# Performance work log

Hardware: AMD Instinct MI355X
Metric: run time of the kernel (lower is better)

## Reference

```python
import jax, jax.numpy as jnp
import numpy as np

EMB_DIM = 768
NUM_HEADS = 12
HEAD_DIM = EMB_DIM // NUM_HEADS
B, S = 8, 1024


def setup_inputs() -> dict:
    key = jax.random.key(0)
    ks = jax.random.split(key, 8)
    q = jax.random.normal(ks[0], (B, S, EMB_DIM), dtype=jnp.float32)
    k = jax.random.normal(ks[1], (B, S, EMB_DIM), dtype=jnp.float32)
    v = jax.random.normal(ks[2], (B, S, EMB_DIM), dtype=jnp.float32)
    # Per-head projection weights, torch nn.Linear layout [out_dim, in_dim]
    xav = float(np.sqrt(6.0 / (HEAD_DIM + HEAD_DIM)))
    Wq = jax.random.uniform(ks[3], (NUM_HEADS, HEAD_DIM, HEAD_DIM), jnp.float32, -xav, xav)
    Wk = jax.random.uniform(ks[4], (NUM_HEADS, HEAD_DIM, HEAD_DIM), jnp.float32, -xav, xav)
    Wv = jax.random.uniform(ks[5], (NUM_HEADS, HEAD_DIM, HEAD_DIM), jnp.float32, -xav, xav)
    # Output projection (torch Linear default init scale not critical for correctness baseline)
    bound = float(1.0 / np.sqrt(EMB_DIM))
    Wo = jax.random.uniform(ks[6], (EMB_DIM, EMB_DIM), jnp.float32, -bound, bound)
    bo = jax.random.uniform(ks[7], (EMB_DIM,), jnp.float32, -bound, bound)
    return {"q": q, "k": k, "v": v, "Wq": Wq, "Wk": Wk, "Wv": Wv, "Wo": Wo, "bo": bo}


def reference(q, k, v, Wq, Wk, Wv, Wo, bo):
    b, s, _ = q.shape
    # split heads: [B, S, E] -> [B, H, S, d]
    def split(x):
        return x.reshape(b, s, NUM_HEADS, HEAD_DIM).transpose(0, 2, 1, 3)
    qh, kh, vh = split(q), split(k), split(v)
    # per-head linear (torch: y = x @ W^T), vectorized over heads
    Q = jnp.einsum('bhsd,hod->bhso', qh, Wq)
    K = jnp.einsum('bhsd,hod->bhso', kh, Wk)
    V = jnp.einsum('bhsd,hod->bhso', vh, Wv)
    scale = 1.0 / jnp.sqrt(jnp.float32(HEAD_DIM))
    scores = jnp.einsum('bhqd,bhkd->bhqk', Q, K) * scale  # [B,H,S,S]
    weights = jax.nn.softmax(scores, axis=-1)
    attn = jnp.einsum('bhqk,bhkd->bhqd', weights, V)
    # merge heads: [B,H,S,d] -> [B,S,E]
    attn = attn.transpose(0, 2, 1, 3).reshape(b, s, EMB_DIM)
    return attn @ Wo.T + bo
```

## Files before the change

kernel.cpp:

```cpp
#include <hip/hip_runtime.h>
#include <hip/hip_bf16.h>

#define BB 8
#define SS 1024
#define EE 768
#define HH 12
#define DD 64
#define NT (BB*SS)

typedef __attribute__((ext_vector_type(8))) short bf16x8;
typedef __attribute__((ext_vector_type(4))) float f32x4;

__device__ __forceinline__ ushort f2bf(float f) {
  union { float f; unsigned u; } x; x.f = f;
  unsigned r = x.u + 0x7fffu + ((x.u >> 16) & 1u);
  return (ushort)(r >> 16);
}

__device__ __forceinline__ unsigned cvtpk(float a, float b) {
  unsigned r;
  asm("v_cvt_pk_bf16_f32 %0, %1, %2" : "=v"(r) : "v"(a), "v"(b));
  return r;
}

__device__ __forceinline__ void gl2lds(const void* g, void* l) {
  __builtin_amdgcn_global_load_lds(
      (const __attribute__((address_space(1))) unsigned int*)g,
      (__attribute__((address_space(3))) unsigned int*)l, 16, 0, 0);
}

#define MFMA16(A, B, C) __builtin_amdgcn_mfma_f32_16x16x32_bf16((A), (B), (C), 0, 0, 0)

__global__ void cvt_weights(const float* __restrict__ Wq, const float* __restrict__ Wk,
                            const float* __restrict__ Wv, const float* __restrict__ Wo,
                            ushort* __restrict__ Wqb, ushort* __restrict__ Wkb,
                            ushort* __restrict__ Wvb, ushort* __restrict__ Wob) {
  int i = blockIdx.x * blockDim.x + threadIdx.x;
  const int NW = HH*DD*DD;
  if (i < NW) { Wqb[i] = f2bf(Wq[i]); Wkb[i] = f2bf(Wk[i]); Wvb[i] = f2bf(Wv[i]); }
  if (i < EE*EE) Wob[i] = f2bf(Wo[i]);
}

__global__ __launch_bounds__(256) void proj_qkv(
    const float* __restrict__ q, const float* __restrict__ k, const float* __restrict__ v,
    const ushort* __restrict__ Wqb, const ushort* __restrict__ Wkb, const ushort* __restrict__ Wvb,
    ushort* __restrict__ Qb, ushort* __restrict__ Kb, ushort* __restrict__ Vt) {
  int bid = blockIdx.x;
  int m  = bid / (BB*HH*4);
  int r  = bid % (BB*HH*4);
  int bh = r % (BB*HH);
  int tg = r / (BB*HH);
  int b = bh / HH, h = bh % HH;

  int tid = threadIdx.x;
  int w = tid >> 6, l = tid & 63;
  int lr = l & 15, lg = l >> 4;

  const float*  xbase = (m==0 ? q : (m==1 ? k : v))
                      + ((size_t)(b*SS + tg*256 + w*16 + lr))*EE + h*DD;
  const ushort* W = (m==0 ? Wqb : (m==1 ? Wkb : Wvb)) + h*DD*DD;

  bf16x8 wb0[4], wb1[4];
#pragma unroll
  for (int f = 0; f < 4; ++f) {
    wb0[f] = *(const bf16x8*)(W + (f*16 + lr)*DD + lg*8);
    wb1[f] = *(const bf16x8*)(W + (f*16 + lr)*DD + 32 + lg*8);
  }

  f32x4 nx0 = *(const f32x4*)(xbase + lg*8);
  f32x4 nx1 = *(const f32x4*)(xbase + lg*8 + 4);
  f32x4 nx2 = *(const f32x4*)(xbase + 32 + lg*8);
  f32x4 nx3 = *(const f32x4*)(xbase + 36 + lg*8);

  float qscale = (m == 0) ? 0.18033688011112042f : 1.0f;

#pragma unroll
  for (int t = 0; t < 4; ++t) {
    f32x4 c0 = nx0, c1 = nx1, c2 = nx2, c3 = nx3;
    if (t < 3) {
      const float* xn = xbase + (size_t)(t + 1)*64*EE;
      nx0 = *(const f32x4*)(xn + lg*8);
      nx1 = *(const f32x4*)(xn + lg*8 + 4);
      nx2 = *(const f32x4*)(xn + 32 + lg*8);
      nx3 = *(const f32x4*)(xn + 36 + lg*8);
    }
    union { bf16x8 v; unsigned u[4]; } a0, a1;
    a0.u[0] = cvtpk(c0[0], c0[1]); a0.u[1] = cvtpk(c0[2], c0[3]);
    a0.u[2] = cvtpk(c1[0], c1[1]); a0.u[3] = cvtpk(c1[2], c1[3]);
    a1.u[0] = cvtpk(c2[0], c2[1]); a1.u[1] = cvtpk(c2[2], c2[3]);
    a1.u[2] = cvtpk(c3[0], c3[1]); a1.u[3] = cvtpk(c3[2], c3[3]);

    f32x4 acc[4] = {};
    int st = tg*4 + t;
    if (m == 2) {
#pragma unroll
      for (int f = 0; f < 4; ++f) {
        acc[f] = MFMA16(a0.v, wb0[f], acc[f]);
        acc[f] = MFMA16(a1.v, wb1[f], acc[f]);
      }
      int posb = st*64 + 32*(w>>1) + 8*lg + 4*(w&1);
#pragma unroll
      for (int f = 0; f < 4; ++f) {
        ushort2 p0, p1;
        *(unsigned*)&p0 = cvtpk(acc[f][0], acc[f][1]);
        *(unsigned*)&p1 = cvtpk(acc[f][2], acc[f][3]);
        ushort4 pk; pk.x = p0.x; pk.y = p0.y; pk.z = p1.x; pk.w = p1.y;
        *(ushort4*)(Vt + ((size_t)bh*DD + f*16 + lr)*SS + posb) = pk;
      }
    } else {
#pragma unroll
      for (int f = 0; f < 4; ++f) {
        acc[f] = MFMA16(wb0[f], a0.v, acc[f]);
        acc[f] = MFMA16(wb1[f], a1.v, acc[f]);
      }
      ushort* dst = (m == 0 ? Qb : Kb) + ((size_t)bh*SS + st*64 + w*16 + lr)*DD;
#pragma unroll
      for (int f = 0; f < 4; ++f) {
        ushort2 p0, p1;
        *(unsigned*)&p0 = cvtpk(acc[f][0]*qscale, acc[f][1]*qscale);
        *(unsigned*)&p1 = cvtpk(acc[f][2]*qscale, acc[f][3]*qscale);
        ushort4 pk; pk.x = p0.x; pk.y = p0.y; pk.z = p1.x; pk.w = p1.y;
        *(ushort4*)(dst + f*16 + lg*4) = pk;
      }
    }
  }
}

__global__ __launch_bounds__(256) void attn_fwd(
    const ushort* __restrict__ Qb, const ushort* __restrict__ Kb,
    const ushort* __restrict__ Vt, ushort* __restrict__ attn) {
  __shared__ uint4 ldsq[2560];
  char* ldsb = (char*)ldsq;

  int bid = blockIdx.x;
  int bh = bid % (BB*HH);
  int qt = bid / (BB*HH);
  int b = bh / HH, h = bh % HH;
  int tid = threadIdx.x, w = tid >> 6, l = tid & 63;
  int lr = l & 15, lg = l >> 4;

  const ushort* Qp0 = Qb + ((size_t)bh*SS + qt*128 + w*32 + lr)*DD;
  bf16x8 bq[2][2];
  bq[0][0] = *(const bf16x8*)(Qp0 + lg*8);
  bq[0][1] = *(const bf16x8*)(Qp0 + 32 + lg*8);
  bq[1][0] = *(const bf16x8*)(Qp0 + 16*DD + lg*8);
  bq[1][1] = *(const bf16x8*)(Qp0 + 16*DD + 32 + lg*8);

  const ushort* Kbh = Kb + (size_t)bh*SS*DD;
  const ushort* Vbh = Vt + (size_t)bh*DD*SS;

  const short ONE = (short)0x3F80;
  bf16x8 ones = {ONE, ONE, ONE, ONE, ONE, ONE, ONE, ONE};

  f32x4 lsum[2] = {};
  f32x4 o[2][4] = {};

#define STAGE_K(kbuf, kt) do {                                                   \
    char* KB_ = ldsb + (kbuf)*8192;                                              \
    const ushort* ksrc = Kbh + ((size_t)((kt)*64 + w*16 + lr))*DD + lg*8;        \
    gl2lds(ksrc,      KB_ + tid*16);                                             \
    gl2lds(ksrc + 32, KB_ + 4096 + tid*16);                                      \
  } while (0)
#define STAGE_V(vbuf, kt) do {                                                   \
    char* VB_ = ldsb + 24576 + (vbuf)*8192;                                      \
    const ushort* vsrc = Vbh + ((size_t)(w*16 + lr))*SS + (kt)*64 + lg*8;        \
    gl2lds(vsrc,      VB_ + tid*16);                                             \
    gl2lds(vsrc + 32, VB_ + 4096 + tid*16);                                      \
  } while (0)

  STAGE_K(0, 0);
  STAGE_V(0, 0);
  STAGE_K(1, 1);
  int kbuf = 0, vbuf = 0;
  for (int kt = 0; kt < 16; ++kt) {
    const char* KB_ = ldsb + kbuf*8192;
    const char* VB_ = ldsb + 24576 + vbuf*8192;

    if (kt < 15) { asm volatile("s_waitcnt vmcnt(2)" ::: "memory"); }
    else         { asm volatile("s_waitcnt vmcnt(0)" ::: "memory"); }
    __builtin_amdgcn_s_barrier();
    __builtin_amdgcn_sched_barrier(0);

    if (kt < 15) STAGE_V(vbuf ^ 1, kt + 1);
    if (kt < 14) { int nk = kbuf + 2; if (nk >= 3) nk -= 3; STAGE_K(nk, kt + 2); }

    f32x4 st0[4] = {}, st1[4] = {};
    __builtin_amdgcn_s_setprio(1);
#pragma unroll
    for (int f = 0; f < 4; ++f) {
      bf16x8 k0 = *(const bf16x8*)(KB_ + f*1024 + l*16);
      bf16x8 k1 = *(const bf16x8*)(KB_ + 4096 + f*1024 + l*16);
      st0[f] = MFMA16(k0, bq[0][0], st0[f]);
      st0[f] = MFMA16(k1, bq[0][1], st0[f]);
      st1[f] = MFMA16(k0, bq[1][0], st1[f]);
      st1[f] = MFMA16(k1, bq[1][1], st1[f]);
    }
    __builtin_amdgcn_s_setprio(0);

    union { bf16x8 v; unsigned u[4]; } pba[2], pbb[2];
#pragma unroll
    for (int s = 0; s < 2; ++s) {
      f32x4* st = (s == 0) ? st0 : st1;
#pragma unroll
      for (int f = 0; f < 4; ++f) {
#pragma unroll
        for (int j = 0; j < 4; ++j) st[f][j] = __builtin_amdgcn_exp2f(st[f][j]);
      }
      pba[s].u[0] = cvtpk(st[0][0], st[0][1]); pba[s].u[1] = cvtpk(st[0][2], st[0][3]);
      pba[s].u[2] = cvtpk(st[1][0], st[1][1]); pba[s].u[3] = cvtpk(st[1][2], st[1][3]);
      pbb[s].u[0] = cvtpk(st[2][0], st[2][1]); pbb[s].u[1] = cvtpk(st[2][2], st[2][3]);
      pbb[s].u[2] = cvtpk(st[3][0], st[3][1]); pbb[s].u[3] = cvtpk(st[3][2], st[3][3]);
    }

    __builtin_amdgcn_s_setprio(1);
#pragma unroll
    for (int f = 0; f < 4; ++f) {
      bf16x8 va = *(const bf16x8*)(VB_ + f*1024 + l*16);
      bf16x8 vc = *(const bf16x8*)(VB_ + 4096 + f*1024 + l*16);
      o[0][f] = MFMA16(va, pba[0].v, o[0][f]);
      o[0][f] = MFMA16(vc, pbb[0].v, o[0][f]);
      o[1][f] = MFMA16(va, pba[1].v, o[1][f]);
      o[1][f] = MFMA16(vc, pbb[1].v, o[1][f]);
    }
    lsum[0] = MFMA16(ones, pba[0].v, lsum[0]);
    lsum[0] = MFMA16(ones, pbb[0].v, lsum[0]);
    lsum[1] = MFMA16(ones, pba[1].v, lsum[1]);
    lsum[1] = MFMA16(ones, pbb[1].v, lsum[1]);
    __builtin_amdgcn_s_setprio(0);

    kbuf = (kbuf == 2) ? 0 : kbuf + 1;
    vbuf ^= 1;
  }
#undef STAGE_K
#undef STAGE_V

#pragma unroll
  for (int s = 0; s < 2; ++s) {
    float inv = 1.0f / lsum[s][0];
    ushort* orow = attn + ((size_t)(b*SS + qt*128 + w*32 + s*16 + lr))*EE + h*DD;
#pragma unroll
    for (int f = 0; f < 4; ++f) {
      ushort4 pkd;
      pkd.x = f2bf(o[s][f][0] * inv);
      pkd.y = f2bf(o[s][f][1] * inv);
      pkd.z = f2bf(o[s][f][2] * inv);
      pkd.w = f2bf(o[s][f][3] * inv);
      *(ushort4*)(orow + f*16 + lg*4) = pkd;
    }
  }
}

__global__ __launch_bounds__(256) void out_proj(
    const ushort* __restrict__ attn, const ushort* __restrict__ Wob,
    const float* __restrict__ bo, float* __restrict__ out) {
  __shared__ uint4 ldsq[3072];
  char* ldsb = (char*)ldsq;

  int bid = blockIdx.x;
  int mt = bid & 127;
  int nt = bid >> 7;
  int tid = threadIdx.x, w = tid >> 6, l = tid & 63;
  int lr = l & 15, lg = l >> 4;

  int rS = tid >> 3;
  int cSw = (((tid & 7) * 16) ^ ((rS & 7) << 4)) >> 1;

  const ushort* Abase = attn + ((size_t)mt*64)*EE;
  const ushort* Bbase = Wob + ((size_t)nt*128)*EE;

#define OSTAGE(bufidx, kt) do {                                                  \
    char* LA_ = ldsb + (bufidx)*24576;                                           \
    char* LB_ = LA_ + 8192;                                                      \
    const ushort* asrc = Abase + (kt)*64 + cSw;                                  \
    const ushort* bsrc = Bbase + (kt)*64 + cSw;                                  \
    gl2lds(asrc + (size_t)rS*EE,        LA_ + tid*16);                           \
    gl2lds(asrc + (size_t)(rS+32)*EE,   LA_ + 4096 + tid*16);                    \
    gl2lds(bsrc + (size_t)rS*EE,        LB_ + tid*16);                           \
    gl2lds(bsrc + (size_t)(rS+32)*EE,   LB_ + 4096 + tid*16);                    \
    gl2lds(bsrc + (size_t)(rS+64)*EE,   LB_ + 8192 + tid*16);                    \
    gl2lds(bsrc + (size_t)(rS+96)*EE,   LB_ + 12288 + tid*16);                   \
  } while (0)

  f32x4 acc[4][2] = {};

#define OCOMPUTE(bufidx) do {                                                    \
    const char* LA_ = ldsb + (bufidx)*24576;                                     \
    const char* LB_ = LA_ + 8192;                                                \
    bf16x8 af[4][2], bf[2][2];                                                   \
    _Pragma("unroll")                                                            \
    for (int f = 0; f < 4; ++f) {                                                \
      int row = f*16 + lr; int sw = (row & 7) << 4;                              \
      af[f][0] = *(const bf16x8*)(LA_ + row*128 + ((lg*16) ^ sw));               \
      af[f][1] = *(const bf16x8*)(LA_ + row*128 + ((64 + lg*16) ^ sw));          \
    }                                                                            \
    _Pragma("unroll")                                                            \
    for (int g = 0; g < 2; ++g) {                                                \
      int row = w*32 + g*16 + lr; int sw = (row & 7) << 4;                       \
      bf[g][0] = *(const bf16x8*)(LB_ + row*128 + ((lg*16) ^ sw));               \
      bf[g][1] = *(const bf16x8*)(LB_ + row*128 + ((64 + lg*16) ^ sw));          \
    }                                                                            \
    _Pragma("unroll")                                                            \
    for (int f = 0; f < 4; ++f) {                                                \
      _Pragma("unroll")                                                          \
      for (int g = 0; g < 2; ++g) {                                              \
        acc[f][g] = MFMA16(af[f][0], bf[g][0], acc[f][g]);                       \
        acc[f][g] = MFMA16(af[f][1], bf[g][1], acc[f][g]);                       \
      }                                                                          \
    }                                                                            \
  } while (0)

  OSTAGE(0, 0);
  for (int kt = 0; kt < EE/64; ++kt) {
    if (kt < EE/64 - 1) OSTAGE((kt + 1) & 1, kt + 1);
    if (kt < EE/64 - 1) { asm volatile("s_waitcnt vmcnt(6)" ::: "memory"); }
    else                { asm volatile("s_waitcnt vmcnt(0)" ::: "memory"); }
    __builtin_amdgcn_s_barrier();
    __builtin_amdgcn_sched_barrier(0);
    OCOMPUTE(kt & 1);
    __builtin_amdgcn_s_barrier();
    __builtin_amdgcn_sched_barrier(0);
  }
#undef OSTAGE
#undef OCOMPUTE

#pragma unroll
  for (int g = 0; g < 2; ++g) {
    int col = nt*128 + w*32 + g*16 + lr;
    float bias = bo[col];
#pragma unroll
    for (int f = 0; f < 4; ++f) {
#pragma unroll
      for (int j = 0; j < 4; ++j) {
        int row = mt*64 + f*16 + lg*4 + j;
        out[(size_t)row*EE + col] = acc[f][g][j] + bias;
      }
    }
  }
}

extern "C" void kernel_launch(void* const* d_in, const int* in_sizes, int n_in,
                              void* d_out, int out_size, void* d_ws, size_t ws_size,
                              hipStream_t stream) {
  (void)in_sizes; (void)n_in; (void)out_size; (void)ws_size;
  const float* q  = (const float*)d_in[0];
  const float* k  = (const float*)d_in[1];
  const float* v  = (const float*)d_in[2];
  const float* Wq = (const float*)d_in[3];
  const float* Wk = (const float*)d_in[4];
  const float* Wv = (const float*)d_in[5];
  const float* Wo = (const float*)d_in[6];
  const float* bo = (const float*)d_in[7];
  float* out = (float*)d_out;

  char* ws = (char*)d_ws;
  const size_t SZ = (size_t)BB*HH*SS*DD*2;
  ushort* Qb   = (ushort*)(ws);
  ushort* Kb   = (ushort*)(ws + SZ);
  ushort* Vt   = (ushort*)(ws + 2*SZ);
  ushort* attn = (ushort*)(ws + 3*SZ);
  ushort* Wqb  = (ushort*)(ws + 4*SZ);
  ushort* Wkb  = (ushort*)(ws + 4*SZ +   98304);
  ushort* Wvb  = (ushort*)(ws + 4*SZ + 2*98304);
  ushort* Wob  = (ushort*)(ws + 4*SZ + 3*98304);

  cvt_weights<<<(EE*EE + 255)/256, 256, 0, stream>>>(Wq, Wk, Wv, Wo, Wqb, Wkb, Wvb, Wob);
  proj_qkv<<<3*BB*HH*4, 256, 0, stream>>>(q, k, v, Wqb, Wkb, Wvb, Qb, Kb, Vt);
  attn_fwd<<<BB*HH*(SS/128), 256, 0, stream>>>(Qb, Kb, Vt, attn);
  out_proj<<<(NT/64)*(EE/128), 256, 0, stream>>>(attn, Wob, bo, out);
}
```

Before: 82.53 us.

## Fold weight conversion into QKV projection kernel and deepen input prefetch

Removes the separate cvt_weights launch. Per-head Wq/Wk/Wv are now converted from fp32 to bf16 in registers inside proj_qkv, and extra blocks appended to the proj_qkv grid convert Wo with vectorized packed conversions. The input prefetch in proj_qkv is also made two tiles deep instead of one. This saves one kernel launch and a global round trip for the small weights, at the cost of each block rereading fp32 weights and holding more live registers.

Result: faster. 79.64 us, median of 2 (-3.5%).

```diff
diff --git a/kernel.cpp b/kernel.cpp
--- a/kernel.cpp
+++ b/kernel.cpp
@@ -31,58 +31,76 @@
 
 #define MFMA16(A, B, C) __builtin_amdgcn_mfma_f32_16x16x32_bf16((A), (B), (C), 0, 0, 0)
 
-__global__ void cvt_weights(const float* __restrict__ Wq, const float* __restrict__ Wk,
-                            const float* __restrict__ Wv, const float* __restrict__ Wo,
-                            ushort* __restrict__ Wqb, ushort* __restrict__ Wkb,
-                            ushort* __restrict__ Wvb, ushort* __restrict__ Wob) {
-  int i = blockIdx.x * blockDim.x + threadIdx.x;
-  const int NW = HH*DD*DD;
-  if (i < NW) { Wqb[i] = f2bf(Wq[i]); Wkb[i] = f2bf(Wk[i]); Wvb[i] = f2bf(Wv[i]); }
-  if (i < EE*EE) Wob[i] = f2bf(Wo[i]);
-}
-
 __global__ __launch_bounds__(256) void proj_qkv(
     const float* __restrict__ q, const float* __restrict__ k, const float* __restrict__ v,
-    const ushort* __restrict__ Wqb, const ushort* __restrict__ Wkb, const ushort* __restrict__ Wvb,
-    ushort* __restrict__ Qb, ushort* __restrict__ Kb, ushort* __restrict__ Vt) {
+    const float* __restrict__ Wq, const float* __restrict__ Wk, const float* __restrict__ Wv,
+    const float* __restrict__ Wo,
+    ushort* __restrict__ Qb, ushort* __restrict__ Kb, ushort* __restrict__ Vt,
+    ushort* __restrict__ Wob) {
   int bid = blockIdx.x;
+  int tid = threadIdx.x;
+
+  if (bid >= 3*BB*HH*4) {
+    int i = (bid - 3*BB*HH*4) * 2048 + tid * 8;
+    f32x4 w0 = *(const f32x4*)(Wo + i);
+    f32x4 w1 = *(const f32x4*)(Wo + i + 4);
+    uint4 pk;
+    pk.x = cvtpk(w0[0], w0[1]);
+    pk.y = cvtpk(w0[2], w0[3]);
+    pk.z = cvtpk(w1[0], w1[1]);
+    pk.w = cvtpk(w1[2], w1[3]);
+    *(uint4*)(Wob + i) = pk;
+    return;
+  }
+
   int m  = bid / (BB*HH*4);
   int r  = bid % (BB*HH*4);
   int bh = r % (BB*HH);
   int tg = r / (BB*HH);
   int b = bh / HH, h = bh % HH;
 
-  int tid = threadIdx.x;
   int w = tid >> 6, l = tid & 63;
   int lr = l & 15, lg = l >> 4;
 
-  const float*  xbase = (m==0 ? q : (m==1 ? k : v))
-                      + ((size_t)(b*SS + tg*256 + w*16 + lr))*EE + h*DD;
-  const ushort* W = (m==0 ? Wqb : (m==1 ? Wkb : Wvb)) + h*DD*DD;
+  const float* xbase = (m==0 ? q : (m==1 ? k : v))
+                     + ((size_t)(b*SS + tg*256 + w*16 + lr))*EE + h*DD;
+  const float* Wf = (m==0 ? Wq : (m==1 ? Wk : Wv)) + h*DD*DD;
 
   bf16x8 wb0[4], wb1[4];
 #pragma unroll
   for (int f = 0; f < 4; ++f) {
-    wb0[f] = *(const bf16x8*)(W + (f*16 + lr)*DD + lg*8);
-    wb1[f] = *(const bf16x8*)(W + (f*16 + lr)*DD + 32 + lg*8);
-  }
-
-  f32x4 nx0 = *(const f32x4*)(xbase + lg*8);
-  f32x4 nx1 = *(const f32x4*)(xbase + lg*8 + 4);
-  f32x4 nx2 = *(const f32x4*)(xbase + 32 + lg*8);
-  f32x4 nx3 = *(const f32x4*)(xbase + 36 + lg*8);
+    const float* wr = Wf + (f*16 + lr)*DD + lg*8;
+    f32x4 u0 = *(const f32x4*)(wr);      f32x4 u1 = *(const f32x4*)(wr + 4);
+    f32x4 u2 = *(const f32x4*)(wr + 32); f32x4 u3 = *(const f32x4*)(wr + 36);
+    union { bf16x8 v; unsigned u[4]; } t0, t1;
+    t0.u[0] = cvtpk(u0[0], u0[1]); t0.u[1] = cvtpk(u0[2], u0[3]);
+    t0.u[2] = cvtpk(u1[0], u1[1]); t0.u[3] = cvtpk(u1[2], u1[3]);
+    t1.u[0] = cvtpk(u2[0], u2[1]); t1.u[1] = cvtpk(u2[2], u2[3]);
+    t1.u[2] = cvtpk(u3[0], u3[1]); t1.u[3] = cvtpk(u3[2], u3[3]);
+    wb0[f] = t0.v; wb1[f] = t1.v;
+  }
+
+  f32x4 px[2][4];
+#pragma unroll
+  for (int d = 0; d < 2; ++d) {
+    const float* xn = xbase + (size_t)d*64*EE;
+    px[d][0] = *(const f32x4*)(xn + lg*8);
+    px[d][1] = *(const f32x4*)(xn + lg*8 + 4);
+    px[d][2] = *(const f32x4*)(xn + 32 + lg*8);
+    px[d][3] = *(const f32x4*)(xn + 36 + lg*8);
+  }
 
   float qscale = (m == 0) ? 0.18033688011112042f : 1.0f;
 
 #pragma unroll
   for (int t = 0; t < 4; ++t) {
-    f32x4 c0 = nx0, c1 = nx1, c2 = nx2, c3 = nx3;
-    if (t < 3) {
-      const float* xn = xbase + (size_t)(t + 1)*64*EE;
-      nx0 = *(const f32x4*)(xn + lg*8);
-      nx1 = *(const f32x4*)(xn + lg*8 + 4);
-      nx2 = *(const f32x4*)(xn + 32 + lg*8);
-      nx3 = *(const f32x4*)(xn + 36 + lg*8);
+    f32x4 c0 = px[t&1][0], c1 = px[t&1][1], c2 = px[t&1][2], c3 = px[t&1][3];
+    if (t < 2) {
+      const float* xn = xbase + (size_t)(t + 2)*64*EE;
+      px[t&1][0] = *(const f32x4*)(xn + lg*8);
+      px[t&1][1] = *(const f32x4*)(xn + lg*8 + 4);
+      px[t&1][2] = *(const f32x4*)(xn + 32 + lg*8);
+      px[t&1][3] = *(const f32x4*)(xn + 36 + lg*8);
     }
     union { bf16x8 v; unsigned u[4]; } a0, a1;
     a0.u[0] = cvtpk(c0[0], c0[1]); a0.u[1] = cvtpk(c0[2], c0[3]);
@@ -358,13 +376,10 @@
   ushort* Kb   = (ushort*)(ws + SZ);
   ushort* Vt   = (ushort*)(ws + 2*SZ);
   ushort* attn = (ushort*)(ws + 3*SZ);
-  ushort* Wqb  = (ushort*)(ws + 4*SZ);
-  ushort* Wkb  = (ushort*)(ws + 4*SZ +   98304);
-  ushort* Wvb  = (ushort*)(ws + 4*SZ + 2*98304);
-  ushort* Wob  = (ushort*)(ws + 4*SZ + 3*98304);
-
-  cvt_weights<<<(EE*EE + 255)/256, 256, 0, stream>>>(Wq, Wk, Wv, Wo, Wqb, Wkb, Wvb, Wob);
-  proj_qkv<<<3*BB*HH*4, 256, 0, stream>>>(q, k, v, Wqb, Wkb, Wvb, Qb, Kb, Vt);
+  ushort* Wob  = (ushort*)(ws + 4*SZ);
+
+  proj_qkv<<<3*BB*HH*4 + (EE*EE)/2048, 256, 0, stream>>>(
+      q, k, v, Wq, Wk, Wv, Wo, Qb, Kb, Vt, Wob);
   attn_fwd<<<BB*HH*(SS/128), 256, 0, stream>>>(Qb, Kb, Vt, attn);
   out_proj<<<(NT/64)*(EE/128), 256, 0, stream>>>(attn, Wob, bo, out);
 }
```
